# Kernel optimization log

Hardware: AMD Instinct MI355X
Metric: run time of the kernel (lower is better)

The kernel has to match this reference:

```python
import jax, jax.numpy as jnp
import numpy as np

B, T, F, U, OUT_STEPS = 512, 128, 64, 1024, 24


def setup_inputs() -> dict:
    key = jax.random.key(0)
    k0, k1, k2, k3 = jax.random.split(key, 4)
    return {
        "inputs": jax.random.normal(k0, (B, T, F), jnp.float32),
        "Wx": jax.random.normal(k1, (F, 4 * U), jnp.float32) * 0.05,   # input kernel, gates [i|f|g|o]
        "Wh": jax.random.normal(k2, (U, 4 * U), jnp.float32) * 0.02,   # recurrent kernel
        "b": jnp.zeros((4 * U,), jnp.float32),
        "Wd": jax.random.normal(k3, (U, F), jnp.float32) * 0.03,       # Dense readout
        "bd": jnp.zeros((F,), jnp.float32),
    }


def _lstm_step(h, c, x, Wx, Wh, b):
    # Keras LSTMCell: gate order i, f, g(candidate), o; sigmoid recurrent act, tanh act.
    z = x @ Wx + h @ Wh + b                      # [B, 4U]
    i, f, g, o = jnp.split(z, 4, axis=-1)
    i = jax.nn.sigmoid(i)
    f = jax.nn.sigmoid(f)
    g = jnp.tanh(g)
    o = jax.nn.sigmoid(o)
    c_new = f * c + i * g
    h_new = o * jnp.tanh(c_new)
    return h_new, c_new


def reference(inputs, Wx, Wh, b, Wd, bd):
    Bq = inputs.shape[0]
    Uq = Wh.shape[0]
    h0 = jnp.zeros((Bq, Uq), inputs.dtype)
    c0 = jnp.zeros((Bq, Uq), inputs.dtype)

    # ---- warmup: run full LSTM over the input window, keep final state ----
    def warm(carry, x_t):
        h, c = carry
        h, c = _lstm_step(h, c, x_t, Wx, Wh, b)
        return (h, c), None

    (h, c), _ = jax.lax.scan(warm, (h0, c0), jnp.swapaxes(inputs, 0, 1))  # scan over time
    pred = h @ Wd + bd                            # first prediction [B, F]

    def decode(carry, _):
        h, c, p = carry
        h, c = _lstm_step(h, c, p, Wx, Wh, b)
        p = h @ Wd + bd
        return (h, c, p), p

    _, rest = jax.lax.scan(decode, (h, c, pred), None, length=OUT_STEPS - 1)
    preds = jnp.concatenate([pred[None], rest], axis=0)   # [OUT_STEPS, B, F]
    return jnp.swapaxes(preds, 0, 1)                       # [B, OUT_STEPS, F]
```

## Files before the change

### kernel.cpp

```cpp
#include <hip/hip_runtime.h>
#include <math.h>

#define Bq 512
#define Tq 128
#define Fq 64
#define Uq 1024
#define OSTEPS 24
#define NKC16 68

typedef _Float16 f16x8 __attribute__((ext_vector_type(8)));
typedef _Float16 f16x4 __attribute__((ext_vector_type(4)));
typedef _Float16 f16x2 __attribute__((ext_vector_type(2)));
typedef float f32x16 __attribute__((ext_vector_type(16)));
typedef float f32x4 __attribute__((ext_vector_type(4)));
typedef float f32x2 __attribute__((ext_vector_type(2)));

__device__ __forceinline__ float sigmoidf_(float x) {
    return 1.0f / (1.0f + __expf(-x));
}
__device__ __forceinline__ float tanhf_(float x) {
    return 2.0f / (1.0f + __expf(-2.0f * x)) - 1.0f;
}

#define BAR() do {                                             \
    asm volatile("s_waitcnt lgkmcnt(0)" ::: "memory");         \
    __builtin_amdgcn_s_barrier();                              \
} while (0)

__global__ __launch_bounds__(256)
void pack_w(const float* __restrict__ Wh, const float* __restrict__ Wx,
            f16x8* __restrict__ BpH)
{
    long id = (long)blockIdx.x * 256 + threadIdx.x;
    int lane = (int)(id & 63);
    long rest = id >> 6;
    int kc16 = (int)(rest % NKC16);
    int gcol = (int)(rest / NKC16);
    int col = (gcol >> 5) * Uq + (gcol & 31) * 32 + (lane & 31);
    int k0 = kc16 * 16 + (lane >> 5) * 8;
    f16x8 hv;
#pragma unroll
    for (int j = 0; j < 8; ++j) {
        int k = k0 + j;
        float v = (k < Uq) ? Wh[(size_t)k * (4 * Uq) + col]
                           : Wx[(size_t)(k - Uq) * (4 * Uq) + col];
        hv[j] = (_Float16)v;
    }
    BpH[id] = hv;
}

#define STAGE_LOAD(c, j) do {                                                   \
    if ((c) < 16) {                                                             \
        ash[j] = *(const f16x8*)(hrow + (c) * 64);                              \
    } else {                                                                    \
        f32x4 v0_ = *(const f32x4*)xrow;                                        \
        f32x4 v1_ = *(const f32x4*)(xrow + 4);                                  \
        f16x8 hv_;                                                              \
        _Pragma("unroll")                                                       \
        for (int j_ = 0; j_ < 4; ++j_) {                                        \
            hv_[j_]     = (_Float16)v0_[j_];                                    \
            hv_[4 + j_] = (_Float16)v1_[j_];                                    \
        }                                                                       \
        ash[j] = hv_;                                                           \
    }                                                                           \
} while (0)

#define STAGE_WRITE(nb, j) do {                                                 \
    As2[nb][smh][sslot] = ash[j];                                               \
} while (0)

#define LOADB(s, c) do {                                                        \
    Bh[s][0] = bpH0[((c) * 4 + kq) * 64];                                       \
    Bh[s][1] = bpH1[((c) * 4 + kq) * 64];                                       \
} while (0)

#define COMPUTE(cb, si) do {                                                    \
    f16x8 ah0_ = As2[cb][0][rdslot];                                            \
    f16x8 ah1_ = As2[cb][1][rdslot];                                            \
    __builtin_amdgcn_s_setprio(1);                                              \
    _Pragma("unroll")                                                           \
    for (int g2_ = 0; g2_ < 2; ++g2_) {                                         \
        acc[g2_][0] = __builtin_amdgcn_mfma_f32_32x32x16_f16(ah0_, Bh[si][g2_], acc[g2_][0], 0, 0, 0); \
        acc[g2_][1] = __builtin_amdgcn_mfma_f32_32x32x16_f16(ah1_, Bh[si][g2_], acc[g2_][1], 0, 0, 0); \
    }                                                                           \
    __builtin_amdgcn_s_setprio(0);                                              \
} while (0)

__global__ __launch_bounds__(512, 2)
void lstm_step(const _Float16* __restrict__ h_in,
               const float* __restrict__ xsrc,
               long xstride,
               const f16x8* __restrict__ BpH,
               const float* __restrict__ bias,
               _Float16* __restrict__ h_out,
               float* __restrict__ c_st)
{
    __shared__ __align__(16) char smem[4 * 4 * 32 * 36 * 4];
    f16x8 (*As2)[2][256] = (f16x8 (*)[2][256])smem;
    float (*zsd)[4][32][36] = (float (*)[4][32][36])smem;

    const int tid = threadIdx.x;
    const int l   = tid & 63;
    const int w   = tid >> 6;
    const int gp  = w & 1;
    const int kq  = w >> 1;
    const int bm  = (int)blockIdx.x >> 5;
    const int bu  = (int)blockIdx.x & 31;
    const int row0 = bm * 64;

    const int srow = tid >> 3;
    const int kg8  = tid & 7;
    const int smh  = srow >> 5;
    const int sr31 = srow & 31;
    const int sslot = sr31 * 8 + (kg8 ^ (sr31 & 7));

    const int rdslot = (l & 31) * 8 + ((kq * 2 + (l >> 5)) ^ (l & 7));

    const f16x8* bpH0 = BpH + ((size_t)((gp * 2 + 0) * 32 + bu) * NKC16) * 64 + l;
    const f16x8* bpH1 = BpH + ((size_t)((gp * 2 + 1) * 32 + bu) * NKC16) * 64 + l;
    const _Float16* hrow = h_in + (size_t)(row0 + srow) * Uq + kg8 * 8;
    const float*    xrow = xsrc + (size_t)(row0 + srow) * xstride + kg8 * 8;

    f32x16 acc[2][2];
#pragma unroll
    for (int i = 0; i < 16; ++i) {
        acc[0][0][i] = 0.0f; acc[0][1][i] = 0.0f;
        acc[1][0][i] = 0.0f; acc[1][1][i] = 0.0f;
    }

    f16x8 Bh[3][2];
    f16x8 ash[2];

    STAGE_LOAD(0, 0);
    STAGE_LOAD(1, 1);
    LOADB(0, 0);
    LOADB(1, 1);
    STAGE_WRITE(0, 0);
    BAR();

#pragma unroll
    for (int i = 0; i < 17; ++i) {
        if (i <= 14) {
            LOADB((i + 2) % 3, i + 2);
            STAGE_LOAD(i + 2, i & 1);
        }
        if (i <= 15) STAGE_WRITE((i + 1) & 1, (i + 1) & 1);
        COMPUTE(i & 1, i % 3);
        if (i < 16) BAR();
    }

    BAR();

#pragma unroll
    for (int mh = 0; mh < 2; ++mh) {
#pragma unroll
        for (int g2 = 0; g2 < 2; ++g2)
#pragma unroll
            for (int r = 0; r < 16; ++r) {
                int rowi = (r & 3) + 8 * (r >> 2) + 4 * (l >> 5);
                zsd[kq][gp * 2 + g2][rowi][l & 31] = acc[g2][mh][r];
            }
        BAR();
        {
            const int row = tid >> 4;
            const int uu  = (tid & 15) * 2;
            const int grow = row0 + mh * 32 + row;
            const int gu   = bu * 32 + uu;
            const size_t gidx = (size_t)grow * Uq + gu;
            float z[4][2];
#pragma unroll
            for (int g = 0; g < 4; ++g) {
#pragma unroll
                for (int j = 0; j < 2; ++j)
                    z[g][j] = zsd[0][g][row][uu + j] + zsd[1][g][row][uu + j]
                            + zsd[2][g][row][uu + j] + zsd[3][g][row][uu + j];
            }
            f32x2 cv = *(const f32x2*)(c_st + gidx);
            f16x2 hh;
#pragma unroll
            for (int j = 0; j < 2; ++j) {
                float vi = sigmoidf_(z[0][j] + bias[0 * Uq + gu + j]);
                float vf = sigmoidf_(z[1][j] + bias[1 * Uq + gu + j]);
                float vg = tanhf_  (z[2][j] + bias[2 * Uq + gu + j]);
                float vo = sigmoidf_(z[3][j] + bias[3 * Uq + gu + j]);
                float cn = vf * cv[j] + vi * vg;
                cv[j] = cn;
                hh[j] = (_Float16)(vo * tanhf_(cn));
            }
            *(f32x2*)(c_st + gidx) = cv;
            *(f16x2*)(h_out + gidx) = hh;
        }
        if (mh == 0) BAR();
    }
}

__global__ __launch_bounds__(256)
void readout(const _Float16* __restrict__ h, const float* __restrict__ Wd,
             const float* __restrict__ bd, float* __restrict__ p,
             float* __restrict__ out, int step)
{
    __shared__ float red[2][4][64];
    const int t = threadIdx.x;
    const int f = t & 63, kq = t >> 6;
    const int r0 = blockIdx.x * 2;
    float s0 = 0.0f, s1 = 0.0f;
    const _Float16* h0 = h + (size_t)r0 * Uq + kq * 256;
    const float* wp = Wd + (size_t)kq * 256 * Fq + f;
#pragma unroll 4
    for (int i = 0; i < 32; ++i) {
        f16x8 ah = *(const f16x8*)(h0 + i * 8);
        f16x8 bh = *(const f16x8*)(h0 + Uq + i * 8);
#pragma unroll
        for (int j = 0; j < 8; ++j) {
            float wv = wp[(size_t)(i * 8 + j) * Fq];
            s0 = fmaf((float)ah[j], wv, s0);
            s1 = fmaf((float)bh[j], wv, s1);
        }
    }
    red[0][kq][f] = s0;
    red[1][kq][f] = s1;
    __syncthreads();
    if (t < 128) {
        int rr = t >> 6, ff = t & 63;
        float s = red[rr][0][ff] + red[rr][1][ff] + red[rr][2][ff] + red[rr][3][ff] + bd[ff];
        p[(size_t)(r0 + rr) * Fq + ff] = s;
        out[((size_t)(r0 + rr) * OSTEPS + step) * Fq + ff] = s;
    }
}

__global__ void zero_ws(f32x4* __restrict__ a, int n) {
    int i = blockIdx.x * 256 + threadIdx.x;
    f32x4 z = {0.0f, 0.0f, 0.0f, 0.0f};
    if (i < n) a[i] = z;
}

extern "C" void kernel_launch(void* const* d_in, const int* in_sizes, int n_in,
                              void* d_out, int out_size, void* d_ws, size_t ws_size,
                              hipStream_t stream) {
    const float* inputs = (const float*)d_in[0];
    const float* Wx     = (const float*)d_in[1];
    const float* Wh     = (const float*)d_in[2];
    const float* b      = (const float*)d_in[3];
    const float* Wd     = (const float*)d_in[4];
    const float* bd     = (const float*)d_in[5];
    float* out = (float*)d_out;

    float* ws = (float*)d_ws;
    float* c_st = ws;
    _Float16* H0 = (_Float16*)(ws + Bq * Uq);
    _Float16* H1 = H0 + Bq * Uq;
    float* p = (float*)(H1 + Bq * Uq);
    f16x8* BpH = (f16x8*)(p + Bq * Fq);

    pack_w<<<2176, 256, 0, stream>>>(Wh, Wx, BpH);
    zero_ws<<<768, 256, 0, stream>>>((f32x4*)ws, 196608);

    _Float16 *h_c = H0, *h_n = H1;
    for (int t = 0; t < Tq; ++t) {
        lstm_step<<<256, 512, 0, stream>>>(h_c, inputs + (size_t)t * Fq, (long)Tq * Fq,
                                           BpH, b, h_n, c_st);
        _Float16* tmp = h_c; h_c = h_n; h_n = tmp;
    }
    readout<<<Bq / 2, 256, 0, stream>>>(h_c, Wd, bd, p, out, 0);
    for (int s = 1; s < OSTEPS; ++s) {
        lstm_step<<<256, 512, 0, stream>>>(h_c, p, (long)Fq, BpH, b, h_n, c_st);
        _Float16* tmp = h_c; h_c = h_n; h_n = tmp;
        readout<<<Bq / 2, 256, 0, stream>>>(h_c, Wd, bd, p, out, s);
    }
}
```

Baseline: 1.754 ms.

## Halve LSTM step row tile to 32 rows, doubling grid to 512 blocks

```diff
diff --git a/kernel.cpp b/kernel.cpp
--- a/kernel.cpp
+++ b/kernel.cpp
@@ -50,23 +50,25 @@
 }
 
 #define STAGE_LOAD(c, j) do {                                                   \
-    if ((c) < 16) {                                                             \
-        ash[j] = *(const f16x8*)(hrow + (c) * 64);                              \
-    } else {                                                                    \
-        f32x4 v0_ = *(const f32x4*)xrow;                                        \
-        f32x4 v1_ = *(const f32x4*)(xrow + 4);                                  \
-        f16x8 hv_;                                                              \
-        _Pragma("unroll")                                                       \
-        for (int j_ = 0; j_ < 4; ++j_) {                                        \
-            hv_[j_]     = (_Float16)v0_[j_];                                    \
-            hv_[4 + j_] = (_Float16)v1_[j_];                                    \
+    if (tid < 256) {                                                            \
+        if ((c) < 16) {                                                         \
+            ash[j] = *(const f16x8*)(hrow + (c) * 64);                          \
+        } else {                                                                \
+            f32x4 v0_ = *(const f32x4*)xrow;                                    \
+            f32x4 v1_ = *(const f32x4*)(xrow + 4);                              \
+            f16x8 hv_;                                                          \
+            _Pragma("unroll")                                                   \
+            for (int j_ = 0; j_ < 4; ++j_) {                                    \
+                hv_[j_]     = (_Float16)v0_[j_];                                \
+                hv_[4 + j_] = (_Float16)v1_[j_];                                \
+            }                                                                   \
+            ash[j] = hv_;                                                       \
         }                                                                       \
-        ash[j] = hv_;                                                           \
     }                                                                           \
 } while (0)
 
 #define STAGE_WRITE(nb, j) do {                                                 \
-    As2[nb][smh][sslot] = ash[j];                                               \
+    if (tid < 256) As2[nb][sslot] = ash[j];                                     \
 } while (0)
 
 #define LOADB(s, c) do {                                                        \
@@ -75,18 +77,14 @@
 } while (0)
 
 #define COMPUTE(cb, si) do {                                                    \
-    f16x8 ah0_ = As2[cb][0][rdslot];                                            \
-    f16x8 ah1_ = As2[cb][1][rdslot];                                            \
+    f16x8 ah_ = As2[cb][rdslot];                                                \
     __builtin_amdgcn_s_setprio(1);                                              \
-    _Pragma("unroll")                                                           \
-    for (int g2_ = 0; g2_ < 2; ++g2_) {                                         \
-        acc[g2_][0] = __builtin_amdgcn_mfma_f32_32x32x16_f16(ah0_, Bh[si][g2_], acc[g2_][0], 0, 0, 0); \
-        acc[g2_][1] = __builtin_amdgcn_mfma_f32_32x32x16_f16(ah1_, Bh[si][g2_], acc[g2_][1], 0, 0, 0); \
-    }                                                                           \
+    acc[0] = __builtin_amdgcn_mfma_f32_32x32x16_f16(ah_, Bh[si][0], acc[0], 0, 0, 0); \
+    acc[1] = __builtin_amdgcn_mfma_f32_32x32x16_f16(ah_, Bh[si][1], acc[1], 0, 0, 0); \
     __builtin_amdgcn_s_setprio(0);                                              \
 } while (0)
 
-__global__ __launch_bounds__(512, 2)
+__global__ __launch_bounds__(512, 4)
 void lstm_step(const _Float16* __restrict__ h_in,
                const float* __restrict__ xsrc,
                long xstride,
@@ -96,7 +94,7 @@
                float* __restrict__ c_st)
 {
     __shared__ __align__(16) char smem[4 * 4 * 32 * 36 * 4];
-    f16x8 (*As2)[2][256] = (f16x8 (*)[2][256])smem;
+    f16x8 (*As2)[256] = (f16x8 (*)[256])smem;
     float (*zsd)[4][32][36] = (float (*)[4][32][36])smem;
 
     const int tid = threadIdx.x;
@@ -106,13 +104,11 @@
     const int kq  = w >> 1;
     const int bm  = (int)blockIdx.x >> 5;
     const int bu  = (int)blockIdx.x & 31;
-    const int row0 = bm * 64;
-
-    const int srow = tid >> 3;
+    const int row0 = bm * 32;
+
+    const int srow = (tid & 255) >> 3;
     const int kg8  = tid & 7;
-    const int smh  = srow >> 5;
-    const int sr31 = srow & 31;
-    const int sslot = sr31 * 8 + (kg8 ^ (sr31 & 7));
+    const int sslot = srow * 8 + (kg8 ^ (srow & 7));
 
     const int rdslot = (l & 31) * 8 + ((kq * 2 + (l >> 5)) ^ (l & 7));
 
@@ -121,12 +117,9 @@
     const _Float16* hrow = h_in + (size_t)(row0 + srow) * Uq + kg8 * 8;
     const float*    xrow = xsrc + (size_t)(row0 + srow) * xstride + kg8 * 8;
 
-    f32x16 acc[2][2];
-#pragma unroll
-    for (int i = 0; i < 16; ++i) {
-        acc[0][0][i] = 0.0f; acc[0][1][i] = 0.0f;
-        acc[1][0][i] = 0.0f; acc[1][1][i] = 0.0f;
-    }
+    f32x16 acc[2];
+#pragma unroll
+    for (int i = 0; i < 16; ++i) { acc[0][i] = 0.0f; acc[1][i] = 0.0f; }
 
     f16x8 Bh[3][2];
     f16x8 ash[2];
@@ -152,45 +145,41 @@
     BAR();
 
 #pragma unroll
-    for (int mh = 0; mh < 2; ++mh) {
-#pragma unroll
-        for (int g2 = 0; g2 < 2; ++g2)
-#pragma unroll
-            for (int r = 0; r < 16; ++r) {
-                int rowi = (r & 3) + 8 * (r >> 2) + 4 * (l >> 5);
-                zsd[kq][gp * 2 + g2][rowi][l & 31] = acc[g2][mh][r];
-            }
-        BAR();
-        {
-            const int row = tid >> 4;
-            const int uu  = (tid & 15) * 2;
-            const int grow = row0 + mh * 32 + row;
-            const int gu   = bu * 32 + uu;
-            const size_t gidx = (size_t)grow * Uq + gu;
-            float z[4][2];
-#pragma unroll
-            for (int g = 0; g < 4; ++g) {
-#pragma unroll
-                for (int j = 0; j < 2; ++j)
-                    z[g][j] = zsd[0][g][row][uu + j] + zsd[1][g][row][uu + j]
-                            + zsd[2][g][row][uu + j] + zsd[3][g][row][uu + j];
-            }
-            f32x2 cv = *(const f32x2*)(c_st + gidx);
-            f16x2 hh;
-#pragma unroll
-            for (int j = 0; j < 2; ++j) {
-                float vi = sigmoidf_(z[0][j] + bias[0 * Uq + gu + j]);
-                float vf = sigmoidf_(z[1][j] + bias[1 * Uq + gu + j]);
-                float vg = tanhf_  (z[2][j] + bias[2 * Uq + gu + j]);
-                float vo = sigmoidf_(z[3][j] + bias[3 * Uq + gu + j]);
-                float cn = vf * cv[j] + vi * vg;
-                cv[j] = cn;
-                hh[j] = (_Float16)(vo * tanhf_(cn));
-            }
-            *(f32x2*)(c_st + gidx) = cv;
-            *(f16x2*)(h_out + gidx) = hh;
-        }
-        if (mh == 0) BAR();
+    for (int g2 = 0; g2 < 2; ++g2)
+#pragma unroll
+        for (int r = 0; r < 16; ++r) {
+            int rowi = (r & 3) + 8 * (r >> 2) + 4 * (l >> 5);
+            zsd[kq][gp * 2 + g2][rowi][l & 31] = acc[g2][r];
+        }
+    BAR();
+    {
+        const int row = tid >> 4;
+        const int uu  = (tid & 15) * 2;
+        const int grow = row0 + row;
+        const int gu   = bu * 32 + uu;
+        const size_t gidx = (size_t)grow * Uq + gu;
+        float z[4][2];
+#pragma unroll
+        for (int g = 0; g < 4; ++g) {
+#pragma unroll
+            for (int j = 0; j < 2; ++j)
+                z[g][j] = zsd[0][g][row][uu + j] + zsd[1][g][row][uu + j]
+                        + zsd[2][g][row][uu + j] + zsd[3][g][row][uu + j];
+        }
+        f32x2 cv = *(const f32x2*)(c_st + gidx);
+        f16x2 hh;
+#pragma unroll
+        for (int j = 0; j < 2; ++j) {
+            float vi = sigmoidf_(z[0][j] + bias[0 * Uq + gu + j]);
+            float vf = sigmoidf_(z[1][j] + bias[1 * Uq + gu + j]);
+            float vg = tanhf_  (z[2][j] + bias[2 * Uq + gu + j]);
+            float vo = sigmoidf_(z[3][j] + bias[3 * Uq + gu + j]);
+            float cn = vf * cv[j] + vi * vg;
+            cv[j] = cn;
+            hh[j] = (_Float16)(vo * tanhf_(cn));
+        }
+        *(f32x2*)(c_st + gidx) = cv;
+        *(f16x2*)(h_out + gidx) = hh;
     }
 }
 
@@ -257,13 +246,13 @@
 
     _Float16 *h_c = H0, *h_n = H1;
     for (int t = 0; t < Tq; ++t) {
-        lstm_step<<<256, 512, 0, stream>>>(h_c, inputs + (size_t)t * Fq, (long)Tq * Fq,
+        lstm_step<<<512, 512, 0, stream>>>(h_c, inputs + (size_t)t * Fq, (long)Tq * Fq,
                                            BpH, b, h_n, c_st);
         _Float16* tmp = h_c; h_c = h_n; h_n = tmp;
     }
     readout<<<Bq / 2, 256, 0, stream>>>(h_c, Wd, bd, p, out, 0);
     for (int s = 1; s < OSTEPS; ++s) {
-        lstm_step<<<256, 512, 0, stream>>>(h_c, p, (long)Fq, BpH, b, h_n, c_st);
+        lstm_step<<<512, 512, 0, stream>>>(h_c, p, (long)Fq, BpH, b, h_n, c_st);
         _Float16* tmp = h_c; h_c = h_n; h_n = tmp;
         readout<<<Bq / 2, 256, 0, stream>>>(h_c, Wd, bd, p, out, s);
     }
```

Result: slower. 1.942 ms (+10.8%).

## Stage four K-chunks per barrier and preload x tile separately

Applied to the files above, without the earlier changes.

```diff
diff --git a/kernel.cpp b/kernel.cpp
--- a/kernel.cpp
+++ b/kernel.cpp
@@ -9,7 +9,6 @@
 #define NKC16 68
 
 typedef _Float16 f16x8 __attribute__((ext_vector_type(8)));
-typedef _Float16 f16x4 __attribute__((ext_vector_type(4)));
 typedef _Float16 f16x2 __attribute__((ext_vector_type(2)));
 typedef float f32x16 __attribute__((ext_vector_type(16)));
 typedef float f32x4 __attribute__((ext_vector_type(4)));
@@ -49,41 +48,38 @@
     BpH[id] = hv;
 }
 
-#define STAGE_LOAD(c, j) do {                                                   \
-    if ((c) < 16) {                                                             \
-        ash[j] = *(const f16x8*)(hrow + (c) * 64);                              \
-    } else {                                                                    \
-        f32x4 v0_ = *(const f32x4*)xrow;                                        \
-        f32x4 v1_ = *(const f32x4*)(xrow + 4);                                  \
-        f16x8 hv_;                                                              \
-        _Pragma("unroll")                                                       \
-        for (int j_ = 0; j_ < 4; ++j_) {                                        \
-            hv_[j_]     = (_Float16)v0_[j_];                                    \
-            hv_[4 + j_] = (_Float16)v1_[j_];                                    \
-        }                                                                       \
-        ash[j] = hv_;                                                           \
+#define STAGE_LOAD4(wl, bank) do {                                              \
+    _Pragma("unroll")                                                           \
+    for (int j_ = 0; j_ < 4; ++j_)                                              \
+        ash[bank][j_] = *(const f16x8*)(hrow + ((wl) * 4 + j_) * 64);           \
+} while (0)
+
+#define STAGE_WRITE4(buf, bank) do {                                            \
+    _Pragma("unroll")                                                           \
+    for (int j_ = 0; j_ < 4; ++j_)                                              \
+        As[buf][j_][smh][sslot] = ash[bank][j_];                                \
+} while (0)
+
+#define LOADB4(slot, wl) do {                                                   \
+    _Pragma("unroll")                                                           \
+    for (int j_ = 0; j_ < 4; ++j_) {                                            \
+        Bh[slot][j_][0] = bpH0[(((wl) * 4 + j_) * 4 + kq) * 64];                \
+        Bh[slot][j_][1] = bpH1[(((wl) * 4 + j_) * 4 + kq) * 64];                \
     }                                                                           \
 } while (0)
 
-#define STAGE_WRITE(nb, j) do {                                                 \
-    As2[nb][smh][sslot] = ash[j];                                               \
-} while (0)
-
-#define LOADB(s, c) do {                                                        \
-    Bh[s][0] = bpH0[((c) * 4 + kq) * 64];                                       \
-    Bh[s][1] = bpH1[((c) * 4 + kq) * 64];                                       \
-} while (0)
-
-#define COMPUTE(cb, si) do {                                                    \
-    f16x8 ah0_ = As2[cb][0][rdslot];                                            \
-    f16x8 ah1_ = As2[cb][1][rdslot];                                            \
-    __builtin_amdgcn_s_setprio(1);                                              \
-    _Pragma("unroll")                                                           \
-    for (int g2_ = 0; g2_ < 2; ++g2_) {                                         \
-        acc[g2_][0] = __builtin_amdgcn_mfma_f32_32x32x16_f16(ah0_, Bh[si][g2_], acc[g2_][0], 0, 0, 0); \
-        acc[g2_][1] = __builtin_amdgcn_mfma_f32_32x32x16_f16(ah1_, Bh[si][g2_], acc[g2_][1], 0, 0, 0); \
+#define COMPUTE4(buf, slot) do {                                                \
+    _Pragma("unroll")                                                           \
+    for (int j_ = 0; j_ < 4; ++j_) {                                            \
+        f16x8 ah0_ = As[buf][j_][0][rdslot];                                    \
+        f16x8 ah1_ = As[buf][j_][1][rdslot];                                    \
+        __builtin_amdgcn_s_setprio(1);                                          \
+        acc[0][0] = __builtin_amdgcn_mfma_f32_32x32x16_f16(ah0_, Bh[slot][j_][0], acc[0][0], 0, 0, 0); \
+        acc[0][1] = __builtin_amdgcn_mfma_f32_32x32x16_f16(ah1_, Bh[slot][j_][0], acc[0][1], 0, 0, 0); \
+        acc[1][0] = __builtin_amdgcn_mfma_f32_32x32x16_f16(ah0_, Bh[slot][j_][1], acc[1][0], 0, 0, 0); \
+        acc[1][1] = __builtin_amdgcn_mfma_f32_32x32x16_f16(ah1_, Bh[slot][j_][1], acc[1][1], 0, 0, 0); \
+        __builtin_amdgcn_s_setprio(0);                                          \
     }                                                                           \
-    __builtin_amdgcn_s_setprio(0);                                              \
 } while (0)
 
 __global__ __launch_bounds__(512, 2)
@@ -95,8 +91,9 @@
                _Float16* __restrict__ h_out,
                float* __restrict__ c_st)
 {
-    __shared__ __align__(16) char smem[4 * 4 * 32 * 36 * 4];
-    f16x8 (*As2)[2][256] = (f16x8 (*)[2][256])smem;
+    __shared__ __align__(16) char smem[73728];
+    f16x8 (*As)[4][2][256] = (f16x8 (*)[4][2][256])smem;
+    f16x8 (*xbuf)[256] = (f16x8 (*)[256])(smem + 65536);
     float (*zsd)[4][32][36] = (float (*)[4][32][36])smem;
 
     const int tid = threadIdx.x;
@@ -128,27 +125,52 @@
         acc[1][0][i] = 0.0f; acc[1][1][i] = 0.0f;
     }
 
-    f16x8 Bh[3][2];
-    f16x8 ash[2];
-
-    STAGE_LOAD(0, 0);
-    STAGE_LOAD(1, 1);
-    LOADB(0, 0);
-    LOADB(1, 1);
-    STAGE_WRITE(0, 0);
-    BAR();
-
-#pragma unroll
-    for (int i = 0; i < 17; ++i) {
-        if (i <= 14) {
-            LOADB((i + 2) % 3, i + 2);
-            STAGE_LOAD(i + 2, i & 1);
+    f16x8 Bh[2][4][2];
+    f16x8 Bx[2];
+    f16x8 ash[2][4];
+
+    {
+        f32x4 v0_ = *(const f32x4*)xrow;
+        f32x4 v1_ = *(const f32x4*)(xrow + 4);
+        f16x8 hv_;
+#pragma unroll
+        for (int j_ = 0; j_ < 4; ++j_) {
+            hv_[j_]     = (_Float16)v0_[j_];
+            hv_[4 + j_] = (_Float16)v1_[j_];
         }
-        if (i <= 15) STAGE_WRITE((i + 1) & 1, (i + 1) & 1);
-        COMPUTE(i & 1, i % 3);
-        if (i < 16) BAR();
-    }
-
+        xbuf[smh][sslot] = hv_;
+    }
+    Bx[0] = bpH0[(64 + kq) * 64];
+    Bx[1] = bpH1[(64 + kq) * 64];
+    STAGE_LOAD4(0, 0);
+    STAGE_LOAD4(1, 1);
+    LOADB4(0, 0);
+    STAGE_WRITE4(0, 0);
+    BAR();
+
+    LOADB4(1, 1);
+    STAGE_LOAD4(2, 0);
+    STAGE_WRITE4(1, 1);
+    COMPUTE4(0, 0);
+    BAR();
+    LOADB4(0, 2);
+    STAGE_LOAD4(3, 1);
+    STAGE_WRITE4(0, 0);
+    COMPUTE4(1, 1);
+    BAR();
+    LOADB4(1, 3);
+    STAGE_WRITE4(1, 1);
+    COMPUTE4(0, 0);
+    BAR();
+    COMPUTE4(1, 1);
+    {
+        f16x8 ah0_ = xbuf[0][rdslot];
+        f16x8 ah1_ = xbuf[1][rdslot];
+        acc[0][0] = __builtin_amdgcn_mfma_f32_32x32x16_f16(ah0_, Bx[0], acc[0][0], 0, 0, 0);
+        acc[0][1] = __builtin_amdgcn_mfma_f32_32x32x16_f16(ah1_, Bx[0], acc[0][1], 0, 0, 0);
+        acc[1][0] = __builtin_amdgcn_mfma_f32_32x32x16_f16(ah0_, Bx[1], acc[1][0], 0, 0, 0);
+        acc[1][1] = __builtin_amdgcn_mfma_f32_32x32x16_f16(ah1_, Bx[1], acc[1][1], 0, 0, 0);
+    }
     BAR();
 
 #pragma unroll
```

Measured after the change: 1.786 ms. Within noise of the previous version (+1.8%).
